# Kernel tuning notes

Hardware: AMD Instinct MI355X
Metric: run time of the kernel (lower is better)

The kernel has to match this reference:

```python
import jax, jax.numpy as jnp
import numpy as np

N, C, H, W = 16, 256, 64, 64
KC, VC, HEADS = 256, 256, 8

def setup_inputs() -> dict:
    key = jax.random.key(0)
    ks = jax.random.split(key, 9)
    s = 0.02
    return {
        "x": jax.random.normal(ks[0], (N, C, H, W), dtype=jnp.float32),
        "Wk": jax.random.normal(ks[1], (KC, C), dtype=jnp.float32) * s,
        "bk": jax.random.normal(ks[2], (KC,), dtype=jnp.float32) * s,
        "Wq": jax.random.normal(ks[3], (KC, C), dtype=jnp.float32) * s,
        "bq": jax.random.normal(ks[4], (KC,), dtype=jnp.float32) * s,
        "Wv": jax.random.normal(ks[5], (VC, C), dtype=jnp.float32) * s,
        "bv": jax.random.normal(ks[6], (VC,), dtype=jnp.float32) * s,
        "Wr": jax.random.normal(ks[7], (C, VC), dtype=jnp.float32) * s,
        "br": jax.random.normal(ks[8], (C,), dtype=jnp.float32) * s,
    }

def reference(x, Wk, bk, Wq, bq, Wv, bv, Wr, br):
    n, c, h, w = x.shape
    hw = h * w
    hk = KC // HEADS   # per-head key channels
    hv = VC // HEADS   # per-head value channels
    # 1x1 convs as channel matmuls
    keys = jnp.einsum('oi,nihw->nohw', Wk, x) + bk[None, :, None, None]
    queries = jnp.einsum('oi,nihw->nohw', Wq, x) + bq[None, :, None, None]
    values = jnp.einsum('oi,nihw->nohw', Wv, x) + bv[None, :, None, None]
    # split heads: (n, heads, ch_per_head, hw)
    k = keys.reshape(n, HEADS, hk, hw)
    q = queries.reshape(n, HEADS, hk, hw)
    v = values.reshape(n, HEADS, hv, hw)
    k = jax.nn.softmax(k, axis=3)   # softmax over spatial positions
    q = jax.nn.softmax(q, axis=2)   # softmax over key channels
    # context: (n, heads, hk, hv)
    ctx = jnp.einsum('nhkl,nhvl->nhkv', k, v)
    # attended: (n, heads, hv, hw)
    att = jnp.einsum('nhkv,nhkl->nhvl', ctx, q)
    agg = att.reshape(n, VC, h, w)
    out = jnp.einsum('ov,nvhw->nohw', Wr, agg) + br[None, :, None, None] + x
    return out
```

## Files before the change

kernel.cpp:

```cpp
#include <hip/hip_runtime.h>

#define NB   16
#define CD   256
#define HWD  4096

typedef __attribute__((ext_vector_type(8))) short short8;
typedef __attribute__((ext_vector_type(4))) float f32x4;

static __device__ __forceinline__ float b2f(unsigned short u) {
  union { unsigned int i; float f; } x; x.i = ((unsigned int)u) << 16; return x.f;
}
static __device__ __forceinline__ unsigned short f2b(float f) {
  union { float f; unsigned int i; } x; x.f = f;
  return (unsigned short)((x.i + 0x7fffu + ((x.i >> 16) & 1u)) >> 16);
}

static __device__ __forceinline__ void gload16(const void* g, const unsigned short* l) {
  __builtin_amdgcn_global_load_lds(
      (const __attribute__((address_space(1))) void*)g,
      (__attribute__((address_space(3))) void*)l, 16, 0, 0);
}

__global__ __launch_bounds__(256)
void prep_kernel(const float* __restrict__ Wk, const float* __restrict__ Wq,
                 const float* __restrict__ Wv, unsigned short* __restrict__ Wc)
{
  int e4 = blockIdx.x * 256 + threadIdx.x;
  int base = e4 * 4;
  int w = base >> 16, off = base & 65535;
  const float* W = (w == 0) ? Wk : (w == 1) ? Wq : Wv;
  f32x4 v = *(const f32x4*)(W + off);
  unsigned int lo = (unsigned int)f2b(v.x) | ((unsigned int)f2b(v.y) << 16);
  unsigned int hi = (unsigned int)f2b(v.z) | ((unsigned int)f2b(v.w) << 16);
  *(uint2*)(Wc + base) = make_uint2(lo, hi);
}

__global__ __launch_bounds__(256)
void xt_kernel(const float* __restrict__ x, unsigned short* __restrict__ xT)
{
  __shared__ __align__(16) unsigned short T[64 * 72];
  const int t = threadIdx.x;
  const int l0 = blockIdx.x * 64, c0 = blockIdx.y * 64, n = blockIdx.z;
  const int l = t & 63, cs = t >> 6;
  const float* xn = x + (size_t)n * CD * HWD;
#pragma unroll
  for (int i = 0; i < 16; ++i) {
    int c = cs + i * 4;
    T[l * 72 + c] = f2b(xn[(size_t)(c0 + c) * HWD + l0 + l]);
  }
  __syncthreads();
  unsigned short* dst = xT + ((size_t)n * HWD + l0) * CD + c0;
#pragma unroll
  for (int i = 0; i < 2; ++i) {
    int e = t + i * 256;
    int lr = e >> 3, c8 = (e & 7) * 8;
    *(short8*)(dst + (size_t)lr * CD + c8) = *(const short8*)(T + lr * 72 + c8);
  }
}

__global__ __launch_bounds__(256, 2)
void kqv_kernel(const unsigned short* __restrict__ Wc,
                const unsigned short* __restrict__ xT,
                const float* __restrict__ bk, const float* __restrict__ bq,
                const float* __restrict__ bv,
                unsigned short* __restrict__ keys,
                unsigned short* __restrict__ qsm,
                unsigned short* __restrict__ vals)
{
  __shared__ __align__(16) unsigned short smem[17408];
  unsigned short* As = smem;
  unsigned short* Bs = smem + 8192;

  const int t  = threadIdx.x;
  const int lt = blockIdx.x;
  const int mt = blockIdx.y;
  const int n  = blockIdx.z;
  const int l0 = lt * 128;
  const int m0 = mt * 128;
  const int wsel = m0 >> 8;
  const int ocbase = m0 & 255;

  const unsigned short* Ag  = Wc;
  const unsigned short* Btn = xT + (size_t)n * HWD * CD;

  const int w = t >> 6, lane = t & 63;
  const int wr = (w >> 1) * 64, wc = (w & 1) * 64;
  const int lhi = lane >> 4, llo = lane & 15;

  f32x4 acc[4][4] = {};

  const int srow = t >> 3, sslot = (t & 7) * 8;
  for (int ks = 0; ks < 4; ++ks) {
    const int k0 = ks * 64;
#pragma unroll
    for (int i = 0; i < 4; ++i) {
      int row = srow + i * 32;
      gload16(Ag + (size_t)(m0 + row) * CD + k0 + sslot, As + (t + i * 256) * 8);
      gload16(Btn + (size_t)(l0 + row) * CD + k0 + sslot, Bs + (t + i * 256) * 8);
    }
    __syncthreads();
#pragma unroll
    for (int kk = 0; kk < 2; ++kk) {
      const int koff = kk * 32 + lhi * 8;
      short8 a[4], b[4];
#pragma unroll
      for (int mi = 0; mi < 4; ++mi)
        a[mi] = *(const short8*)(As + (wr + mi * 16 + llo) * 64 + koff);
#pragma unroll
      for (int ni = 0; ni < 4; ++ni)
        b[ni] = *(const short8*)(Bs + (wc + ni * 16 + llo) * 64 + koff);
#pragma unroll
      for (int mi = 0; mi < 4; ++mi)
#pragma unroll
        for (int ni = 0; ni < 4; ++ni)
          acc[mi][ni] = __builtin_amdgcn_mfma_f32_16x16x32_bf16(a[mi], b[ni], acc[mi][ni], 0, 0, 0);
    }
    __syncthreads();
  }

  const float* bias = (wsel == 0) ? bk : (wsel == 1) ? bq : bv;
  float breg[4][4];
#pragma unroll
  for (int mi = 0; mi < 4; ++mi)
#pragma unroll
    for (int r = 0; r < 4; ++r)
      breg[mi][r] = bias[ocbase + wr + mi * 16 + lhi * 4 + r];
#pragma unroll
  for (int mi = 0; mi < 4; ++mi)
#pragma unroll
    for (int ni = 0; ni < 4; ++ni)
#pragma unroll
      for (int r = 0; r < 4; ++r)
        acc[mi][ni][r] += breg[mi][r];

  if (wsel == 1) {
#pragma unroll
    for (int g = 0; g < 2; ++g) {
#pragma unroll
      for (int ni = 0; ni < 4; ++ni) {
        float m = -1e30f;
#pragma unroll
        for (int mi = 2 * g; mi < 2 * g + 2; ++mi)
#pragma unroll
          for (int r = 0; r < 4; ++r) m = fmaxf(m, acc[mi][ni][r]);
        m = fmaxf(m, __shfl_xor(m, 16));
        m = fmaxf(m, __shfl_xor(m, 32));
        float s = 0.f;
#pragma unroll
        for (int mi = 2 * g; mi < 2 * g + 2; ++mi)
#pragma unroll
          for (int r = 0; r < 4; ++r) {
            float e = __expf(acc[mi][ni][r] - m);
            acc[mi][ni][r] = e;
            s += e;
          }
        s += __shfl_xor(s, 16);
        s += __shfl_xor(s, 32);
        float inv = 1.f / s;
#pragma unroll
        for (int mi = 2 * g; mi < 2 * g + 2; ++mi)
#pragma unroll
          for (int r = 0; r < 4; ++r) acc[mi][ni][r] *= inv;
      }
    }
  }

  unsigned short* Co = smem;
#pragma unroll
  for (int mi = 0; mi < 4; ++mi)
#pragma unroll
    for (int ni = 0; ni < 4; ++ni) {
      int col = wc + ni * 16 + llo;
#pragma unroll
      for (int r = 0; r < 4; ++r) {
        int row = wr + mi * 16 + lhi * 4 + r;
        Co[row * 136 + col] = f2b(acc[mi][ni][r]);
      }
    }
  __syncthreads();

  unsigned short* dst = ((wsel == 0) ? keys : (wsel == 1) ? qsm : vals)
                        + ((size_t)(n * CD + ocbase)) * HWD + l0;
#pragma unroll
  for (int i = 0; i < 8; ++i) {
    int e = t + i * 256;
    int row = e >> 4, c8 = (e & 15) * 8;
    *(short8*)(dst + (size_t)row * HWD + c8) = *(const short8*)(Co + row * 136 + c8);
  }
}

__global__ __launch_bounds__(256)
void rowstats_kernel(const unsigned short* __restrict__ keys,
                     float* __restrict__ stats)
{
  __shared__ float red[8];
  const int r = blockIdx.x;
  const int t = threadIdx.x;
  const unsigned short* rowp = keys + (size_t)r * HWD;
  float v[16];
  float m = -1e30f;
#pragma unroll
  for (int i = 0; i < 2; ++i) {
    const short8 u = *(const short8*)(rowp + t * 8 + i * 2048);
#pragma unroll
    for (int j = 0; j < 8; ++j) {
      v[i * 8 + j] = b2f((unsigned short)u[j]);
      m = fmaxf(m, v[i * 8 + j]);
    }
  }
#pragma unroll
  for (int off = 1; off < 64; off <<= 1) m = fmaxf(m, __shfl_xor(m, off));
  if ((t & 63) == 0) red[t >> 6] = m;
  __syncthreads();
  m = fmaxf(fmaxf(red[0], red[1]), fmaxf(red[2], red[3]));
  float s = 0.f;
#pragma unroll
  for (int i = 0; i < 16; ++i) s += __expf(v[i] - m);
#pragma unroll
  for (int off = 1; off < 64; off <<= 1) s += __shfl_xor(s, off);
  if ((t & 63) == 0) red[4 + (t >> 6)] = s;
  __syncthreads();
  if (t == 0) {
    s = red[4] + red[5] + red[6] + red[7];
    stats[r * 2]     = m;
    stats[r * 2 + 1] = 1.f / s;
  }
}

__global__ __launch_bounds__(256)
void ctx_kernel(const unsigned short* __restrict__ keys,
                const unsigned short* __restrict__ vals,
                const float* __restrict__ stats,
                float* __restrict__ ctxp)
{
  __shared__ float Cs[4][32][33];
  const int hf = blockIdx.x;
  const int nh = blockIdx.y;
  const int n = nh >> 3, h = nh & 7;
  const int t = threadIdx.x, w = t >> 6, lane = t & 63;
  const int lhi = lane >> 4, llo = lane & 15;
  const int lbase = hf * 2048 + w * 512;

  const unsigned short* kr = keys + (size_t)(n * CD + h * 32) * HWD;
  const unsigned short* vr = vals + (size_t)(n * CD + h * 32) * HWD;

  float mx[2], inv[2];
#pragma unroll
  for (int mi = 0; mi < 2; ++mi) {
    int kc = mi * 16 + llo;
    mx[mi]  = stats[(n * CD + h * 32 + kc) * 2];
    inv[mi] = stats[(n * CD + h * 32 + kc) * 2 + 1];
  }

  f32x4 acc[2][2] = {};
  for (int ks = 0; ks < 16; ++ks) {
    const int loff = lbase + ks * 32 + lhi * 8;
    short8 a[2], b[2];
#pragma unroll
    for (int mi = 0; mi < 2; ++mi) {
      const short8 u = *(const short8*)(kr + (size_t)(mi * 16 + llo) * HWD + loff);
      short8 af;
#pragma unroll
      for (int j = 0; j < 8; ++j)
        af[j] = (short)f2b(__expf(b2f((unsigned short)u[j]) - mx[mi]) * inv[mi]);
      a[mi] = af;
    }
#pragma unroll
    for (int ni = 0; ni < 2; ++ni)
      b[ni] = *(const short8*)(vr + (size_t)(ni * 16 + llo) * HWD + loff);
    acc[0][0] = __builtin_amdgcn_mfma_f32_16x16x32_bf16(a[0], b[0], acc[0][0], 0, 0, 0);
    acc[0][1] = __builtin_amdgcn_mfma_f32_16x16x32_bf16(a[0], b[1], acc[0][1], 0, 0, 0);
    acc[1][0] = __builtin_amdgcn_mfma_f32_16x16x32_bf16(a[1], b[0], acc[1][0], 0, 0, 0);
    acc[1][1] = __builtin_amdgcn_mfma_f32_16x16x32_bf16(a[1], b[1], acc[1][1], 0, 0, 0);
  }

#pragma unroll
  for (int mi = 0; mi < 2; ++mi)
#pragma unroll
    for (int ni = 0; ni < 2; ++ni)
#pragma unroll
      for (int r = 0; r < 4; ++r)
        Cs[w][mi * 16 + lhi * 4 + r][ni * 16 + llo] = acc[mi][ni][r];
  __syncthreads();
#pragma unroll
  for (int i = 0; i < 4; ++i) {
    int e = t + i * 256;
    int kc = e >> 5, vc = e & 31;
    float sum = Cs[0][kc][vc] + Cs[1][kc][vc] + Cs[2][kc][vc] + Cs[3][kc][vc];
    ctxp[((size_t)hf * 128 + nh) * 1024 + e] = sum;
  }
}

__global__ __launch_bounds__(256)
void proj_kernel(const float* __restrict__ ctxp, const float* __restrict__ Wr,
                 unsigned short* __restrict__ M)
{
  __shared__ float cs[32][33];
  const int nh = blockIdx.x;
  const int n = nh >> 3, h = nh & 7;
  const int t = threadIdx.x;
#pragma unroll
  for (int i = 0; i < 4; ++i) {
    int e = t + i * 256;
    cs[e >> 5][e & 31] = ctxp[(size_t)nh * 1024 + e] + ctxp[((size_t)128 + nh) * 1024 + e];
  }
  __syncthreads();
  float wreg[32];
  const float* wp = Wr + (size_t)t * 256 + h * 32;
#pragma unroll
  for (int i = 0; i < 8; ++i) {
    f32x4 v = *(const f32x4*)(wp + i * 4);
    wreg[i * 4] = v.x; wreg[i * 4 + 1] = v.y; wreg[i * 4 + 2] = v.z; wreg[i * 4 + 3] = v.w;
  }
  unsigned short o16[32];
#pragma unroll
  for (int kc = 0; kc < 32; ++kc) {
    float s = 0.f;
#pragma unroll
    for (int vv = 0; vv < 32; ++vv) s += wreg[vv] * cs[kc][vv];
    o16[kc] = f2b(s);
  }
  unsigned short* mp = M + (size_t)(n * CD + t) * 256 + h * 32;
#pragma unroll
  for (int i = 0; i < 8; ++i) {
    unsigned int lo = (unsigned int)o16[i * 4]     | ((unsigned int)o16[i * 4 + 1] << 16);
    unsigned int hi = (unsigned int)o16[i * 4 + 2] | ((unsigned int)o16[i * 4 + 3] << 16);
    *(uint2*)(mp + i * 4) = make_uint2(lo, hi);
  }
}

__global__ __launch_bounds__(256, 2)
void out_kernel(const unsigned short* __restrict__ M,
                const unsigned short* __restrict__ qsm,
                const float* __restrict__ br,
                const float* __restrict__ x,
                float* __restrict__ out)
{
  __shared__ __align__(16) unsigned short As[64 * 264];
  __shared__ __align__(16) unsigned short Bs[64 * 264];
  const int t = threadIdx.x;
  const int lt = blockIdx.x, mt = blockIdx.y, n = blockIdx.z;
  const int l0 = lt * 64, m0 = mt * 64;

  const unsigned short* Mn = M + (size_t)n * CD * 256;
#pragma unroll
  for (int i = 0; i < 8; ++i) {
    int idx = t + i * 256;
    int row = idx >> 5, s8 = (idx & 31) << 3;
    *(short8*)(As + row * 264 + s8) = *(const short8*)(Mn + (size_t)(m0 + row) * 256 + s8);
  }
  const unsigned short* qn = qsm + (size_t)n * CD * HWD;
  {
    int l = t & 63, g0 = t >> 6;
#pragma unroll
    for (int i = 0; i < 16; ++i) {
      int c = (g0 + i * 4) << 2;
      unsigned short q0 = qn[(size_t)(c + 0) * HWD + l0 + l];
      unsigned short q1 = qn[(size_t)(c + 1) * HWD + l0 + l];
      unsigned short q2 = qn[(size_t)(c + 2) * HWD + l0 + l];
      unsigned short q3 = qn[(size_t)(c + 3) * HWD + l0 + l];
      unsigned int lo = (unsigned int)q0 | ((unsigned int)q1 << 16);
      unsigned int hi = (unsigned int)q2 | ((unsigned int)q3 << 16);
      *(uint2*)(Bs + l * 264 + c) = make_uint2(lo, hi);
    }
  }
  __syncthreads();

  const int w = t >> 6, lane = t & 63;
  const int wr = (w >> 1) * 32, wc = (w & 1) * 32;
  const int lhi = lane >> 4, llo = lane & 15;

  f32x4 acc[2][2] = {};
#pragma unroll
  for (int kk = 0; kk < 8; ++kk) {
    const int koff = kk * 32 + lhi * 8;
    short8 a0 = *(const short8*)(As + (wr + llo) * 264 + koff);
    short8 a1 = *(const short8*)(As + (wr + 16 + llo) * 264 + koff);
    short8 b0 = *(const short8*)(Bs + (wc + llo) * 264 + koff);
    short8 b1 = *(const short8*)(Bs + (wc + 16 + llo) * 264 + koff);
    acc[0][0] = __builtin_amdgcn_mfma_f32_16x16x32_bf16(a0, b0, acc[0][0], 0, 0, 0);
    acc[0][1] = __builtin_amdgcn_mfma_f32_16x16x32_bf16(a0, b1, acc[0][1], 0, 0, 0);
    acc[1][0] = __builtin_amdgcn_mfma_f32_16x16x32_bf16(a1, b0, acc[1][0], 0, 0, 0);
    acc[1][1] = __builtin_amdgcn_mfma_f32_16x16x32_bf16(a1, b1, acc[1][1], 0, 0, 0);
  }
  __syncthreads();

  float* Qs = (float*)As;
#pragma unroll
  for (int mi = 0; mi < 2; ++mi)
#pragma unroll
    for (int ni = 0; ni < 2; ++ni)
#pragma unroll
      for (int r = 0; r < 4; ++r) {
        int row = wr + mi * 16 + lhi * 4 + r;
        int col = wc + ni * 16 + llo;
        Qs[row * 65 + col] = acc[mi][ni][r] + br[m0 + row];
      }
  __syncthreads();

  const float* xn = x + (size_t)n * CD * HWD;
  {
    int l = t & 63, r0 = t >> 6;
#pragma unroll
    for (int i = 0; i < 16; ++i) {
      int row = r0 + i * 4;
      size_t off = (size_t)(m0 + row) * HWD + l0 + l;
      out[(size_t)n * CD * HWD + off] = Qs[row * 65 + l] + xn[off];
    }
  }
}

extern "C" void kernel_launch(void* const* d_in, const int* in_sizes, int n_in,
                              void* d_out, int out_size, void* d_ws, size_t ws_size,
                              hipStream_t stream) {
  const float* x  = (const float*)d_in[0];
  const float* Wk = (const float*)d_in[1];
  const float* bk = (const float*)d_in[2];
  const float* Wq = (const float*)d_in[3];
  const float* bq = (const float*)d_in[4];
  const float* Wv = (const float*)d_in[5];
  const float* bv = (const float*)d_in[6];
  const float* Wr = (const float*)d_in[7];
  const float* br = (const float*)d_in[8];
  float* out = (float*)d_out;

  char* ws = (char*)d_ws;
  unsigned short* keys = (unsigned short*)(ws);
  unsigned short* vals = (unsigned short*)(ws + 33554432);
  unsigned short* qsm  = (unsigned short*)(ws + 67108864);
  float* stats         = (float*)(ws + 100663296);
  float* ctxp          = (float*)(ws + 100696064);
  unsigned short* M    = (unsigned short*)(ws + 101744640);
  unsigned short* Wc   = (unsigned short*)(ws + 103841792);
  unsigned short* xT   = (unsigned short*)d_out;

  hipLaunchKernelGGL(prep_kernel, dim3(192), dim3(256), 0, stream, Wk, Wq, Wv, Wc);
  hipLaunchKernelGGL(xt_kernel, dim3(64, 4, NB), dim3(256), 0, stream, x, xT);
  hipLaunchKernelGGL(kqv_kernel, dim3(32, 6, NB), dim3(256), 0, stream,
                     Wc, xT, bk, bq, bv, keys, qsm, vals);
  hipLaunchKernelGGL(rowstats_kernel, dim3(NB * CD), dim3(256), 0, stream, keys, stats);
  hipLaunchKernelGGL(ctx_kernel, dim3(2, 128), dim3(256), 0, stream,
                     keys, vals, stats, ctxp);
  hipLaunchKernelGGL(proj_kernel, dim3(128), dim3(256), 0, stream, ctxp, Wr, M);
  hipLaunchKernelGGL(out_kernel, dim3(64, 4, NB), dim3(256), 0, stream,
                     M, qsm, br, x, out);
}
```

Baseline: 134.8 us.

## Double-buffer KQV GEMM LDS staging and XOR-swizzle tiles

The KQV projection GEMM now uses two LDS buffers, so the global-to-LDS loads for the next K step are issued before the MFMA compute on the current one, which overlaps memory latency with math. The LDS tile layout also gets an XOR swizzle on the 16-byte slot index to reduce bank conflicts on the short8 reads. LDS use per block roughly doubles to 64KB, which may limit occupancy at two blocks per CU. Only one barrier per iteration is kept, and the correctness of the overlap relies on the async loads landing before that barrier.

```diff
diff --git a/kernel.cpp b/kernel.cpp
--- a/kernel.cpp
+++ b/kernel.cpp
@@ -67,9 +67,7 @@
                 unsigned short* __restrict__ qsm,
                 unsigned short* __restrict__ vals)
 {
-  __shared__ __align__(16) unsigned short smem[17408];
-  unsigned short* As = smem;
-  unsigned short* Bs = smem + 8192;
+  __shared__ __align__(16) unsigned short smem[32768];
 
   const int t  = threadIdx.x;
   const int lt = blockIdx.x;
@@ -86,35 +84,51 @@
   const int w = t >> 6, lane = t & 63;
   const int wr = (w >> 1) * 64, wc = (w & 1) * 64;
   const int lhi = lane >> 4, llo = lane & 15;
+  const int rsw = llo & 7;
 
   f32x4 acc[4][4] = {};
 
-  const int srow = t >> 3, sslot = (t & 7) * 8;
-  for (int ks = 0; ks < 4; ++ks) {
+  auto stage = [&](int buf, int ks) {
+    unsigned short* As = smem + buf * 16384;
+    unsigned short* Bs = As + 8192;
     const int k0 = ks * 64;
 #pragma unroll
     for (int i = 0; i < 4; ++i) {
-      int row = srow + i * 32;
-      gload16(Ag + (size_t)(m0 + row) * CD + k0 + sslot, As + (t + i * 256) * 8);
-      gload16(Btn + (size_t)(l0 + row) * CD + k0 + sslot, Bs + (t + i * 256) * 8);
-    }
-    __syncthreads();
+      int s   = t + i * 256;
+      int row = s >> 3;
+      int src = ((s ^ row) & 7) << 3;
+      gload16(Ag  + (size_t)(m0 + row) * CD + k0 + src, As + s * 8);
+      gload16(Btn + (size_t)(l0 + row) * CD + k0 + src, Bs + s * 8);
+    }
+  };
+
+  auto compute = [&](int buf) {
+    const unsigned short* As = smem + buf * 16384;
+    const unsigned short* Bs = As + 8192;
 #pragma unroll
     for (int kk = 0; kk < 2; ++kk) {
-      const int koff = kk * 32 + lhi * 8;
+      const int slot = (kk * 4 + lhi) ^ rsw;
       short8 a[4], b[4];
 #pragma unroll
       for (int mi = 0; mi < 4; ++mi)
-        a[mi] = *(const short8*)(As + (wr + mi * 16 + llo) * 64 + koff);
+        a[mi] = *(const short8*)(As + (wr + mi * 16 + llo) * 64 + slot * 8);
 #pragma unroll
       for (int ni = 0; ni < 4; ++ni)
-        b[ni] = *(const short8*)(Bs + (wc + ni * 16 + llo) * 64 + koff);
+        b[ni] = *(const short8*)(Bs + (wc + ni * 16 + llo) * 64 + slot * 8);
 #pragma unroll
       for (int mi = 0; mi < 4; ++mi)
 #pragma unroll
         for (int ni = 0; ni < 4; ++ni)
           acc[mi][ni] = __builtin_amdgcn_mfma_f32_16x16x32_bf16(a[mi], b[ni], acc[mi][ni], 0, 0, 0);
     }
+  };
+
+  stage(0, 0);
+  __syncthreads();
+#pragma unroll
+  for (int ks = 0; ks < 4; ++ks) {
+    if (ks < 3) stage((ks + 1) & 1, ks + 1);
+    compute(ks & 1);
     __syncthreads();
   }
 
```

After: 130.9 us. -2.9%, faster.
